# Kernel tuning notes

Hardware: AMD Instinct MI355X
Metric: run time of the kernel (lower is better)

## Reference

```python
import jax, jax.numpy as jnp
import numpy as np

B, S, D = 1, 2048, 2048
HQ, HKV, DH = 16, 4, 128
WINDOW = 512  # sliding window encoded in explicit attn_mask


def rotate_half(u):
    u1, u2 = jnp.split(u, 2, axis=-1)
    return jnp.concatenate([-u2, u1], axis=-1)


def setup_inputs() -> dict:
    key = jax.random.key(0)
    ks = jax.random.split(key, 6)
    x = jax.random.normal(ks[0], (B, S, D), dtype=jnp.float32)
    # RoPE caches (standard rotary frequencies, full d_head with duplicated halves)
    pos = jnp.arange(S)
    inv_freq = 1.0 / (10000.0 ** (jnp.arange(0, DH, 2, dtype=jnp.float32) / DH))
    ang = pos[:, None].astype(jnp.float32) * inv_freq[None, :]  # [S, DH/2]
    emb = jnp.concatenate([ang, ang], axis=-1)                  # [S, DH]
    cos_cache = jnp.cos(emb)
    sin_cache = jnp.sin(emb)
    # sliding-window causal mask: attend to j<=i and i-j < WINDOW
    i = jnp.arange(S)[:, None]
    j = jnp.arange(S)[None, :]
    attn_mask = (j <= i) & ((i - j) < WINDOW)
    sc = 0.02
    Wq = jax.random.normal(ks[1], (D, HQ * DH), dtype=jnp.float32) * sc
    Wk = jax.random.normal(ks[2], (D, HKV * DH), dtype=jnp.float32) * sc
    Wv = jax.random.normal(ks[3], (D, HKV * DH), dtype=jnp.float32) * sc
    Wo = jax.random.normal(ks[4], (HQ * DH, D), dtype=jnp.float32) * sc
    return {"x": x, "cos_cache": cos_cache, "sin_cache": sin_cache,
            "positions": pos.astype(jnp.int64), "attn_mask": attn_mask,
            "Wq": Wq, "Wk": Wk, "Wv": Wv, "Wo": Wo}


def reference(x, cos_cache, sin_cache, positions, attn_mask, Wq, Wk, Wv, Wo):
    batch, seq_len, _ = x.shape
    Q = (x @ Wq).reshape(batch, seq_len, HQ, DH).transpose(0, 2, 1, 3)   # [B,HQ,S,DH]
    K = (x @ Wk).reshape(batch, seq_len, HKV, DH).transpose(0, 2, 1, 3)  # [B,HKV,S,DH]
    V = (x @ Wv).reshape(batch, seq_len, HKV, DH).transpose(0, 2, 1, 3)
    # RoPE
    cos = cos_cache[positions][None, None, :, :]  # [1,1,S,DH]
    sin = sin_cache[positions][None, None, :, :]
    Q = Q * cos + rotate_half(Q) * sin
    K = K * cos + rotate_half(K) * sin
    # GQA expansion (repeat_interleave along head dim)
    G = HQ // HKV
    K_exp = jnp.repeat(K, G, axis=1)  # [B,HQ,S,DH]
    V_exp = jnp.repeat(V, G, axis=1)
    scores = jnp.einsum('bhqd,bhkd->bhqk', Q, K_exp) / jnp.sqrt(jnp.float32(DH))
    neg_inf = jnp.finfo(scores.dtype).min
    scores = jnp.where(attn_mask[None, None, :, :], scores, neg_inf)
    weights = jax.nn.softmax(scores, axis=-1)
    attn_out = jnp.einsum('bhqk,bhkd->bhqd', weights, V_exp)
    attn_out = attn_out.transpose(0, 2, 1, 3).reshape(batch, seq_len, HQ * DH)
    output = attn_out @ Wo
    return (output, K, V)  # new kv cache is the (post-RoPE) K, V
```

## Files before the change

kernel.cpp:

```cpp
#include <hip/hip_runtime.h>
#include <stdint.h>

typedef unsigned short u16;
typedef __attribute__((ext_vector_type(4))) float f32x4;
typedef __attribute__((ext_vector_type(8))) short short8;
typedef __attribute__((ext_vector_type(4))) short short4v;

__device__ inline u16 f2bf(float f) {
  union { float f; uint32_t u; } v; v.f = f;
  uint32_t u = v.u;
  u += 0x7fffu + ((u >> 16) & 1u);
  return (u16)(u >> 16);
}
__device__ inline float bf2f(u16 b) {
  union { uint32_t u; float f; } v; v.u = (uint32_t)b << 16; return v.f;
}

__global__ __launch_bounds__(256) void k_prep(const float* __restrict__ x,
                                              const float* __restrict__ Wq, const float* __restrict__ Wk,
                                              const float* __restrict__ Wv, const float* __restrict__ Wo,
                                              u16* __restrict__ xb, u16* __restrict__ WT, u16* __restrict__ WoT) {
  const int b = blockIdx.x, tid = threadIdx.x;
  if (b < 1024) {
    size_t base = (size_t)b * 4096 + tid * 4;
    #pragma unroll
    for (int k = 0; k < 4; ++k) {
      f32x4 v = *(const f32x4*)(x + base + k * 1024);
      short4v o;
      o.x = (short)f2bf(v.x); o.y = (short)f2bf(v.y);
      o.z = (short)f2bf(v.z); o.w = (short)f2bf(v.w);
      *(short4v*)(xb + base + k * 1024) = o;
    }
    return;
  }
  __shared__ float t[64][68];
  const float* W; u16* D; int N, bb;
  if (b < 2048)      { W = Wq; D = WT;                       N = 2048; bb = b - 1024; }
  else if (b < 2304) { W = Wk; D = WT + (size_t)2048 * 2048; N = 512;  bb = b - 2048; }
  else if (b < 2560) { W = Wv; D = WT + (size_t)2560 * 2048; N = 512;  bb = b - 2304; }
  else               { W = Wo; D = WoT;                      N = 2048; bb = b - 2560; }
  const int nb = N >> 6;
  const int n0 = (bb % nb) * 64, k0 = (bb / nb) * 64;
  const int c4 = (tid & 15) * 4, rbase = tid >> 4;
  #pragma unroll
  for (int p = 0; p < 4; ++p) {
    int r = p * 16 + rbase;
    *(f32x4*)&t[r][c4] = *(const f32x4*)&W[(size_t)(k0 + r) * N + n0 + c4];
  }
  __syncthreads();
  const int i = tid >> 2, j = (tid & 3) * 16;
  short8 o0, o1;
  #pragma unroll
  for (int m = 0; m < 8; ++m) o0[m] = (short)f2bf(t[j + m][i]);
  #pragma unroll
  for (int m = 0; m < 8; ++m) o1[m] = (short)f2bf(t[j + 8 + m][i]);
  *(short8*)&D[(size_t)(n0 + i) * 2048 + k0 + j] = o0;
  *(short8*)&D[(size_t)(n0 + i) * 2048 + k0 + j + 8] = o1;
}

__global__ __launch_bounds__(512, 2) void k_gemmqkv(const u16* __restrict__ A,
                                                    const u16* __restrict__ B,
                                                    u16* __restrict__ C) {
  const int K = 2048;
  const int NT = 32;
  __shared__ __align__(16) u16 lds[3 * 20480];
  const int tid = threadIdx.x;
  const int wid = tid >> 6, lane = tid & 63;
  const int quad = lane >> 4, l16 = lane & 15;
  const int wm = (wid >> 2) * 64;
  const int wn = (wid & 3) * 48;
  const int bm = blockIdx.y * 128, bn = blockIdx.x * 192;

  const u16* aSrc[2]; int aDst[2];
  #pragma unroll
  for (int L = 0; L < 2; ++L) {
    int E = (tid + L * 512) * 8;
    int r = E >> 6, pc = (E >> 3) & 7;
    int lc = pc ^ (r & 7);
    aSrc[L] = A + (size_t)(bm + r) * K + lc * 8;
    aDst[L] = E;
  }
  const u16* bSrc[3]; int bDst[3];
  #pragma unroll
  for (int L = 0; L < 3; ++L) {
    int E = (tid + L * 512) * 8;
    int r = E >> 6, pc = (E >> 3) & 7;
    int lc = pc ^ (r & 7);
    bSrc[L] = B + (size_t)(bn + r) * K + lc * 8;
    bDst[L] = 8192 + E;
  }

  #define STAGE(buf, kt) do {                                                              \
    _Pragma("unroll")                                                                      \
    for (int L = 0; L < 2; ++L)                                                            \
      __builtin_amdgcn_global_load_lds(                                                    \
          (const __attribute__((address_space(1))) void*)(aSrc[L] + (kt) * 64),            \
          (__attribute__((address_space(3))) void*)(&lds[(buf) * 20480 + aDst[L]]), 16, 0, 0); \
    _Pragma("unroll")                                                                      \
    for (int L = 0; L < 3; ++L)                                                            \
      __builtin_amdgcn_global_load_lds(                                                    \
          (const __attribute__((address_space(1))) void*)(bSrc[L] + (kt) * 64),            \
          (__attribute__((address_space(3))) void*)(&lds[(buf) * 20480 + bDst[L]]), 16, 0, 0); \
  } while (0)

  f32x4 acc[4][3];
  #pragma unroll
  for (int m = 0; m < 4; ++m)
    #pragma unroll
    for (int n = 0; n < 3; ++n) acc[m][n] = (f32x4){0.f, 0.f, 0.f, 0.f};

  STAGE(0, 0);
  STAGE(1, 1);
  asm volatile("s_waitcnt vmcnt(5)" ::: "memory");
  __builtin_amdgcn_s_barrier();

  int c = 0, p = 2;
  for (int t = 0; t < NT; ++t) {
    if (t + 2 < NT) STAGE(p, t + 2);

    short8 af[4][2], bf[3][2];
    #pragma unroll
    for (int mf = 0; mf < 4; ++mf)
      #pragma unroll
      for (int kc = 0; kc < 2; ++kc) {
        int R = wm + mf * 16 + l16;
        int pc = (kc * 4 + quad) ^ (R & 7);
        af[mf][kc] = *(const short8*)&lds[c * 20480 + R * 64 + pc * 8];
      }
    #pragma unroll
    for (int nf = 0; nf < 3; ++nf)
      #pragma unroll
      for (int kc = 0; kc < 2; ++kc) {
        int Cc = wn + nf * 16 + l16;
        int pc = (kc * 4 + quad) ^ (Cc & 7);
        bf[nf][kc] = *(const short8*)&lds[c * 20480 + 8192 + Cc * 64 + pc * 8];
      }

    __builtin_amdgcn_s_setprio(1);
    #pragma unroll
    for (int mf = 0; mf < 4; ++mf)
      #pragma unroll
      for (int nf = 0; nf < 3; ++nf)
        #pragma unroll
        for (int kc = 0; kc < 2; ++kc)
          acc[mf][nf] = __builtin_amdgcn_mfma_f32_16x16x32_bf16(af[mf][kc], bf[nf][kc], acc[mf][nf], 0, 0, 0);
    __builtin_amdgcn_s_setprio(0);

    if (t + 2 < NT) {
      asm volatile("s_waitcnt vmcnt(5)" ::: "memory");
    } else if (t + 1 < NT) {
      asm volatile("s_waitcnt vmcnt(0)" ::: "memory");
    }
    __builtin_amdgcn_s_barrier();
    c = (c == 2) ? 0 : c + 1;
    p = (p == 2) ? 0 : p + 1;
  }
  #undef STAGE

  #pragma unroll
  for (int mf = 0; mf < 4; ++mf) {
    int row = bm + wm + mf * 16 + quad * 4;
    #pragma unroll
    for (int nf = 0; nf < 3; ++nf) {
      int col = bn + wn + nf * 16 + l16;
      #pragma unroll
      for (int r = 0; r < 4; ++r)
        C[(size_t)(row + r) * 3072 + col] = f2bf(acc[mf][nf][r]);
    }
  }
}

__global__ __launch_bounds__(512, 2) void k_gemmo(const u16* __restrict__ A,
                                                  const u16* __restrict__ B,
                                                  float* __restrict__ C) {
  const int K = 2048;
  const int NT = 32;
  __shared__ __align__(16) u16 lds[3 * 16384];
  const int tid = threadIdx.x;
  const int wid = tid >> 6, lane = tid & 63;
  const int quad = lane >> 4, l16 = lane & 15;
  const int wm = (wid >> 2) * 64;
  const int wn = (wid & 3) * 32;
  const int bm = blockIdx.y * 128, bn = blockIdx.x * 128;

  const u16* aSrc[2]; const u16* bSrc[2]; int dDst[2];
  #pragma unroll
  for (int L = 0; L < 2; ++L) {
    int E = (tid + L * 512) * 8;
    int r = E >> 6, pc = (E >> 3) & 7;
    int lc = pc ^ (r & 7);
    aSrc[L] = A + (size_t)(bm + r) * K + lc * 8;
    bSrc[L] = B + (size_t)(bn + r) * K + lc * 8;
    dDst[L] = E;
  }

  #define STAGEO(buf, kt) do {                                                             \
    _Pragma("unroll")                                                                      \
    for (int L = 0; L < 2; ++L)                                                            \
      __builtin_amdgcn_global_load_lds(                                                    \
          (const __attribute__((address_space(1))) void*)(aSrc[L] + (kt) * 64),            \
          (__attribute__((address_space(3))) void*)(&lds[(buf) * 16384 + dDst[L]]), 16, 0, 0); \
    _Pragma("unroll")                                                                      \
    for (int L = 0; L < 2; ++L)                                                            \
      __builtin_amdgcn_global_load_lds(                                                    \
          (const __attribute__((address_space(1))) void*)(bSrc[L] + (kt) * 64),            \
          (__attribute__((address_space(3))) void*)(&lds[(buf) * 16384 + 8192 + dDst[L]]), 16, 0, 0); \
  } while (0)

  f32x4 acc[4][2];
  #pragma unroll
  for (int m = 0; m < 4; ++m)
    #pragma unroll
    for (int n = 0; n < 2; ++n) acc[m][n] = (f32x4){0.f, 0.f, 0.f, 0.f};

  STAGEO(0, 0);
  STAGEO(1, 1);
  asm volatile("s_waitcnt vmcnt(4)" ::: "memory");
  __builtin_amdgcn_s_barrier();

  int c = 0, p = 2;
  for (int t = 0; t < NT; ++t) {
    if (t + 2 < NT) STAGEO(p, t + 2);

    short8 af[4][2], bf[2][2];
    #pragma unroll
    for (int mf = 0; mf < 4; ++mf)
      #pragma unroll
      for (int kc = 0; kc < 2; ++kc) {
        int R = wm + mf * 16 + l16;
        int pc = (kc * 4 + quad) ^ (R & 7);
        af[mf][kc] = *(const short8*)&lds[c * 16384 + R * 64 + pc * 8];
      }
    #pragma unroll
    for (int nf = 0; nf < 2; ++nf)
      #pragma unroll
      for (int kc = 0; kc < 2; ++kc) {
        int Cc = wn + nf * 16 + l16;
        int pc = (kc * 4 + quad) ^ (Cc & 7);
        bf[nf][kc] = *(const short8*)&lds[c * 16384 + 8192 + Cc * 64 + pc * 8];
      }

    __builtin_amdgcn_s_setprio(1);
    #pragma unroll
    for (int mf = 0; mf < 4; ++mf)
      #pragma unroll
      for (int nf = 0; nf < 2; ++nf)
        #pragma unroll
        for (int kc = 0; kc < 2; ++kc)
          acc[mf][nf] = __builtin_amdgcn_mfma_f32_16x16x32_bf16(af[mf][kc], bf[nf][kc], acc[mf][nf], 0, 0, 0);
    __builtin_amdgcn_s_setprio(0);

    if (t + 2 < NT) {
      asm volatile("s_waitcnt vmcnt(4)" ::: "memory");
    } else if (t + 1 < NT) {
      asm volatile("s_waitcnt vmcnt(0)" ::: "memory");
    }
    __builtin_amdgcn_s_barrier();
    c = (c == 2) ? 0 : c + 1;
    p = (p == 2) ? 0 : p + 1;
  }
  #undef STAGEO

  #pragma unroll
  for (int mf = 0; mf < 4; ++mf) {
    int row = bm + wm + mf * 16 + quad * 4;
    #pragma unroll
    for (int nf = 0; nf < 2; ++nf) {
      int col = bn + wn + nf * 16 + l16;
      #pragma unroll
      for (int r = 0; r < 4; ++r)
        C[(size_t)(row + r) * 2048 + col] = acc[mf][nf][r];
    }
  }
}

__global__ __launch_bounds__(256) void k_post(const u16* __restrict__ P,
                                              const float* __restrict__ cosc, const float* __restrict__ sinc,
                                              u16* __restrict__ Qb, u16* __restrict__ Kb, u16* __restrict__ Vt,
                                              float* __restrict__ Kout, float* __restrict__ Vout) {
  const int b = blockIdx.x, tid = threadIdx.x;
  if (b < 2048) {
    __shared__ float row[3072];
    const int s = b;
    const u16* p0 = P + (size_t)s * 3072;
    for (int i = tid * 4; i < 3072; i += 1024) {
      short4v a0 = *(const short4v*)(p0 + i);
      #pragma unroll
      for (int m = 0; m < 4; ++m)
        row[i + m] = bf2f((u16)a0[m]);
    }
    __syncthreads();
    const int d = tid & 127;
    const int hbase = tid >> 7;
    const float c = cosc[s * 128 + d], sn = sinc[s * 128 + d];
    const float scale = 0.08838834764831845f;
    #pragma unroll
    for (int it = 0; it < 12; ++it) {
      int slice = it * 2 + hbase;
      float v = row[slice * 128 + d];
      if (slice < 20) {
        float other = (d < 64) ? -row[slice * 128 + d + 64] : row[slice * 128 + d - 64];
        float r = v * c + other * sn;
        if (slice < 16) {
          Qb[((size_t)slice * 2048 + s) * 128 + d] = f2bf(r * scale);
        } else {
          int hk = slice - 16;
          Kout[((size_t)hk * 2048 + s) * 128 + d] = r;
          Kb[((size_t)hk * 2048 + s) * 128 + d] = f2bf(r);
        }
      } else {
        int hv = slice - 20;
        Vout[((size_t)hv * 2048 + s) * 128 + d] = v;
      }
    }
  } else {
    __shared__ float t[32][33];
    const int b2 = b - 2048;
    const int c0 = (b2 & 15) * 32, s0 = (b2 >> 4) * 32;
    const int tx = tid & 31, ty = tid >> 5;
    #pragma unroll
    for (int i = ty; i < 32; i += 8) {
      size_t idx = (size_t)(s0 + i) * 3072 + 2560 + c0 + tx;
      t[i][tx] = bf2f(P[idx]);
    }
    __syncthreads();
    const int head = c0 >> 7, dbase = c0 & 127;
    #pragma unroll
    for (int i = ty; i < 32; i += 8)
      Vt[((size_t)head * 128 + dbase + i) * 2048 + s0 + tx] = f2bf(t[tx][i]);
  }
}

__global__ __launch_bounds__(512) void k_attn(const u16* __restrict__ Qb,
                                              const u16* __restrict__ Kb,
                                              const u16* __restrict__ Vt,
                                              u16* __restrict__ O) {
  const int qt = blockIdx.x;
  const int hk = blockIdx.y;
  const int tid = threadIdx.x;
  const int wid = tid >> 6, lane = tid & 63;
  const int quad = lane >> 4, l16 = lane & 15;
  const int h = hk * 4 + (wid >> 1);
  const int qrow0 = qt * 32;
  const int r0 = qrow0 + (wid & 1) * 16;
  const u16* Qh = Qb + (size_t)h * 2048 * 128;
  const u16* Kh = Kb + (size_t)hk * 2048 * 128;
  const u16* Vh = Vt + (size_t)hk * 128 * 2048;

  __shared__ u16 Ks[32 * 136];
  __shared__ u16 Vs[128 * 40];
  __shared__ u16 Ps[8][16 * 40];

  short8 qa[4];
  #pragma unroll
  for (int ks = 0; ks < 4; ++ks)
    qa[ks] = *(const short8*)&Qh[(size_t)(r0 + l16) * 128 + ks * 32 + quad * 8];

  f32x4 o[8];
  #pragma unroll
  for (int dt = 0; dt < 8; ++dt) o[dt] = (f32x4){0.f, 0.f, 0.f, 0.f};
  float lsum[4] = {0.f, 0.f, 0.f, 0.f};

  const int c0 = qrow0 > 511 ? (qrow0 - 511) >> 5 : 0;
  const int c1 = (qrow0 + 31) >> 5;

  short8 kreg, vreg;
  {
    const int jb = c0 * 32;
    kreg = *(const short8*)&Kh[(size_t)(jb + (tid >> 4)) * 128 + (tid & 15) * 8];
    vreg = *(const short8*)&Vh[(size_t)(tid >> 2) * 2048 + jb + (tid & 3) * 8];
  }

  for (int c = c0; c <= c1; ++c) {
    const int jbase = c * 32;
    __syncthreads();
    *(short8*)&Ks[(tid >> 4) * 136 + (tid & 15) * 8] = kreg;
    *(short8*)&Vs[(tid >> 2) * 40  + (tid & 3)  * 8] = vreg;
    if (c < c1) {
      const int jb = jbase + 32;
      kreg = *(const short8*)&Kh[(size_t)(jb + (tid >> 4)) * 128 + (tid & 15) * 8];
      vreg = *(const short8*)&Vh[(size_t)(tid >> 2) * 2048 + jb + (tid & 3) * 8];
    }
    __syncthreads();

    f32x4 sc[2];
    #pragma unroll
    for (int ni = 0; ni < 2; ++ni) {
      sc[ni] = (f32x4){0.f, 0.f, 0.f, 0.f};
      #pragma unroll
      for (int ks = 0; ks < 4; ++ks) {
        short8 kf = *(const short8*)&Ks[(ni * 16 + l16) * 136 + ks * 32 + quad * 8];
        sc[ni] = __builtin_amdgcn_mfma_f32_16x16x32_bf16(qa[ks], kf, sc[ni], 0, 0, 0);
      }
    }
    #pragma unroll
    for (int ni = 0; ni < 2; ++ni) {
      const int jlo = jbase + ni * 16;
      const bool none = (jlo > r0 + 15) || (jlo + 15 < r0 - 511);
      const bool allv = (jlo + 15 <= r0) && (jlo >= r0 - 496);
      float p[4];
      if (none) {
        p[0] = p[1] = p[2] = p[3] = 0.f;
      } else if (allv) {
        #pragma unroll
        for (int r = 0; r < 4; ++r) p[r] = __expf(sc[ni][r]);
      } else {
        const int j = jlo + l16;
        #pragma unroll
        for (int r = 0; r < 4; ++r) {
          int i = r0 + quad * 4 + r;
          bool ok = (j <= i) && (i - j < 512);
          p[r] = ok ? __expf(sc[ni][r]) : 0.f;
        }
      }
      #pragma unroll
      for (int r = 0; r < 4; ++r) {
        lsum[r] += p[r];
        Ps[wid][(quad * 4 + r) * 40 + ni * 16 + l16] = f2bf(p[r]);
      }
    }
    short8 pa = *(const short8*)&Ps[wid][l16 * 40 + quad * 8];
    #pragma unroll
    for (int dt = 0; dt < 8; ++dt) {
      short8 vf = *(const short8*)&Vs[(dt * 16 + l16) * 40 + quad * 8];
      o[dt] = __builtin_amdgcn_mfma_f32_16x16x32_bf16(pa, vf, o[dt], 0, 0, 0);
    }
  }

  #pragma unroll
  for (int off = 1; off < 16; off <<= 1)
    #pragma unroll
    for (int r = 0; r < 4; ++r)
      lsum[r] += __shfl_xor(lsum[r], off, 64);
  float inv[4];
  #pragma unroll
  for (int r = 0; r < 4; ++r) inv[r] = 1.0f / lsum[r];

  #pragma unroll
  for (int dt = 0; dt < 8; ++dt) {
    int col = h * 128 + dt * 16 + l16;
    #pragma unroll
    for (int r = 0; r < 4; ++r) {
      int row = r0 + quad * 4 + r;
      O[(size_t)row * 2048 + col] = f2bf(o[dt][r] * inv[r]);
    }
  }
}

extern "C" void kernel_launch(void* const* d_in, const int* in_sizes, int n_in,
                              void* d_out, int out_size, void* d_ws, size_t ws_size,
                              hipStream_t stream) {
  const float* x    = (const float*)d_in[0];
  const float* cosc = (const float*)d_in[1];
  const float* sinc = (const float*)d_in[2];
  const float* Wq = (const float*)d_in[5];
  const float* Wk = (const float*)d_in[6];
  const float* Wv = (const float*)d_in[7];
  const float* Wo = (const float*)d_in[8];

  char* ws = (char*)d_ws;
  u16*   xb    = (u16*)(ws);
  u16*   O     = (u16*)(ws);
  u16*   WT    = (u16*)(ws + (8u  << 20));
  u16*   WoT   = (u16*)(ws + (20u << 20));
  u16*   Qb    = (u16*)(ws + (28u << 20));
  u16*   Kb    = (u16*)(ws + (36u << 20));
  u16*   Vt    = (u16*)(ws + (38u << 20));
  u16*   QKV   = (u16*)(ws + (40u << 20));

  float* outO = (float*)d_out;
  float* outK = (float*)d_out + 4194304;
  float* outV = (float*)d_out + 5242880;

  k_prep<<<3584, 256, 0, stream>>>(x, Wq, Wk, Wv, Wo, xb, WT, WoT);
  k_gemmqkv<<<dim3(16, 16), 512, 0, stream>>>(xb, WT, QKV);
  k_post<<<3072, 256, 0, stream>>>(QKV, cosc, sinc, Qb, Kb, Vt, outK, outV);
  k_attn<<<dim3(64, 4), 512, 0, stream>>>(Qb, Kb, Vt, O);
  k_gemmo<<<dim3(16, 16), 512, 0, stream>>>(O, WoT, outO);
}
```

Measured before the change: 102.4 us.

## Retile output GEMM to 4 waves with BK=32 and double attention KV chunk

The output-projection GEMM moves from 8 waves with a 64-wide K step to 4 waves, each computing a 64x64 tile over a 32-wide K step with a re-derived LDS swizzle. This halves LDS use and increases per-wave register reuse, but doubles the number of barriers and pipeline iterations. Separately, the attention kernel processes 64 keys per chunk instead of 32, halving the number of synchronised load/compute iterations. The cost is more registers and LDS per block and more masked work at the window edges.

```diff
diff --git a/kernel.cpp b/kernel.cpp
--- a/kernel.cpp
+++ b/kernel.cpp
@@ -170,25 +170,24 @@
   }
 }
 
-__global__ __launch_bounds__(512, 2) void k_gemmo(const u16* __restrict__ A,
-                                                  const u16* __restrict__ B,
-                                                  float* __restrict__ C) {
+__global__ __launch_bounds__(256) void k_gemmo(const u16* __restrict__ A,
+                                               const u16* __restrict__ B,
+                                               float* __restrict__ C) {
   const int K = 2048;
-  const int NT = 32;
-  __shared__ __align__(16) u16 lds[3 * 16384];
+  const int NT = 64;
+  __shared__ __align__(16) u16 lds[3 * 8192];
   const int tid = threadIdx.x;
   const int wid = tid >> 6, lane = tid & 63;
   const int quad = lane >> 4, l16 = lane & 15;
-  const int wm = (wid >> 2) * 64;
-  const int wn = (wid & 3) * 32;
+  const int wm = (wid >> 1) * 64, wn = (wid & 1) * 64;
   const int bm = blockIdx.y * 128, bn = blockIdx.x * 128;
 
   const u16* aSrc[2]; const u16* bSrc[2]; int dDst[2];
   #pragma unroll
   for (int L = 0; L < 2; ++L) {
-    int E = (tid + L * 512) * 8;
-    int r = E >> 6, pc = (E >> 3) & 7;
-    int lc = pc ^ (r & 7);
+    int E = (tid + L * 256) * 8;
+    int r = E >> 5, pc = (E >> 3) & 3;
+    int lc = pc ^ ((r >> 1) & 3);
     aSrc[L] = A + (size_t)(bm + r) * K + lc * 8;
     bSrc[L] = B + (size_t)(bn + r) * K + lc * 8;
     dDst[L] = E;
@@ -198,20 +197,20 @@
     _Pragma("unroll")                                                                      \
     for (int L = 0; L < 2; ++L)                                                            \
       __builtin_amdgcn_global_load_lds(                                                    \
-          (const __attribute__((address_space(1))) void*)(aSrc[L] + (kt) * 64),            \
-          (__attribute__((address_space(3))) void*)(&lds[(buf) * 16384 + dDst[L]]), 16, 0, 0); \
+          (const __attribute__((address_space(1))) void*)(aSrc[L] + (kt) * 32),            \
+          (__attribute__((address_space(3))) void*)(&lds[(buf) * 8192 + dDst[L]]), 16, 0, 0); \
     _Pragma("unroll")                                                                      \
     for (int L = 0; L < 2; ++L)                                                            \
       __builtin_amdgcn_global_load_lds(                                                    \
-          (const __attribute__((address_space(1))) void*)(bSrc[L] + (kt) * 64),            \
-          (__attribute__((address_space(3))) void*)(&lds[(buf) * 16384 + 8192 + dDst[L]]), 16, 0, 0); \
+          (const __attribute__((address_space(1))) void*)(bSrc[L] + (kt) * 32),            \
+          (__attribute__((address_space(3))) void*)(&lds[(buf) * 8192 + 4096 + dDst[L]]), 16, 0, 0); \
   } while (0)
 
-  f32x4 acc[4][2];
+  f32x4 acc[4][4];
   #pragma unroll
   for (int m = 0; m < 4; ++m)
     #pragma unroll
-    for (int n = 0; n < 2; ++n) acc[m][n] = (f32x4){0.f, 0.f, 0.f, 0.f};
+    for (int n = 0; n < 4; ++n) acc[m][n] = (f32x4){0.f, 0.f, 0.f, 0.f};
 
   STAGEO(0, 0);
   STAGEO(1, 1);
@@ -222,32 +221,26 @@
   for (int t = 0; t < NT; ++t) {
     if (t + 2 < NT) STAGEO(p, t + 2);
 
-    short8 af[4][2], bf[2][2];
+    short8 af[4], bf[4];
+    #pragma unroll
+    for (int mf = 0; mf < 4; ++mf) {
+      int R = wm + mf * 16 + l16;
+      int pc = quad ^ ((R >> 1) & 3);
+      af[mf] = *(const short8*)&lds[c * 8192 + R * 32 + pc * 8];
+    }
+    #pragma unroll
+    for (int nf = 0; nf < 4; ++nf) {
+      int Cc = wn + nf * 16 + l16;
+      int pc = quad ^ ((Cc >> 1) & 3);
+      bf[nf] = *(const short8*)&lds[c * 8192 + 4096 + Cc * 32 + pc * 8];
+    }
+
+    __builtin_amdgcn_s_setprio(1);
     #pragma unroll
     for (int mf = 0; mf < 4; ++mf)
       #pragma unroll
-      for (int kc = 0; kc < 2; ++kc) {
-        int R = wm + mf * 16 + l16;
-        int pc = (kc * 4 + quad) ^ (R & 7);
-        af[mf][kc] = *(const short8*)&lds[c * 16384 + R * 64 + pc * 8];
-      }
-    #pragma unroll
-    for (int nf = 0; nf < 2; ++nf)
-      #pragma unroll
-      for (int kc = 0; kc < 2; ++kc) {
-        int Cc = wn + nf * 16 + l16;
-        int pc = (kc * 4 + quad) ^ (Cc & 7);
-        bf[nf][kc] = *(const short8*)&lds[c * 16384 + 8192 + Cc * 64 + pc * 8];
-      }
-
-    __builtin_amdgcn_s_setprio(1);
-    #pragma unroll
-    for (int mf = 0; mf < 4; ++mf)
-      #pragma unroll
-      for (int nf = 0; nf < 2; ++nf)
-        #pragma unroll
-        for (int kc = 0; kc < 2; ++kc)
-          acc[mf][nf] = __builtin_amdgcn_mfma_f32_16x16x32_bf16(af[mf][kc], bf[nf][kc], acc[mf][nf], 0, 0, 0);
+      for (int nf = 0; nf < 4; ++nf)
+        acc[mf][nf] = __builtin_amdgcn_mfma_f32_16x16x32_bf16(af[mf], bf[nf], acc[mf][nf], 0, 0, 0);
     __builtin_amdgcn_s_setprio(0);
 
     if (t + 2 < NT) {
@@ -265,7 +258,7 @@
   for (int mf = 0; mf < 4; ++mf) {
     int row = bm + wm + mf * 16 + quad * 4;
     #pragma unroll
-    for (int nf = 0; nf < 2; ++nf) {
+    for (int nf = 0; nf < 4; ++nf) {
       int col = bn + wn + nf * 16 + l16;
       #pragma unroll
       for (int r = 0; r < 4; ++r)
@@ -347,9 +340,9 @@
   const u16* Kh = Kb + (size_t)hk * 2048 * 128;
   const u16* Vh = Vt + (size_t)hk * 128 * 2048;
 
-  __shared__ u16 Ks[32 * 136];
-  __shared__ u16 Vs[128 * 40];
-  __shared__ u16 Ps[8][16 * 40];
+  __shared__ u16 Ks[64 * 136];
+  __shared__ u16 Vs[128 * 72];
+  __shared__ u16 Ps[8][16 * 72];
 
   short8 qa[4];
   #pragma unroll
@@ -361,31 +354,43 @@
   for (int dt = 0; dt < 8; ++dt) o[dt] = (f32x4){0.f, 0.f, 0.f, 0.f};
   float lsum[4] = {0.f, 0.f, 0.f, 0.f};
 
-  const int c0 = qrow0 > 511 ? (qrow0 - 511) >> 5 : 0;
-  const int c1 = (qrow0 + 31) >> 5;
-
-  short8 kreg, vreg;
+  const int c0 = qrow0 > 511 ? (qrow0 - 511) >> 6 : 0;
+  const int c1 = (qrow0 + 31) >> 6;
+
+  short8 kreg[2], vreg[2];
   {
-    const int jb = c0 * 32;
-    kreg = *(const short8*)&Kh[(size_t)(jb + (tid >> 4)) * 128 + (tid & 15) * 8];
-    vreg = *(const short8*)&Vh[(size_t)(tid >> 2) * 2048 + jb + (tid & 3) * 8];
+    const int jb = c0 * 64;
+    #pragma unroll
+    for (int i = 0; i < 2; ++i) {
+      int lin = i * 512 + tid;
+      kreg[i] = *(const short8*)&Kh[(size_t)(jb + (lin >> 4)) * 128 + (lin & 15) * 8];
+      vreg[i] = *(const short8*)&Vh[(size_t)(lin >> 3) * 2048 + jb + (lin & 7) * 8];
+    }
   }
 
   for (int c = c0; c <= c1; ++c) {
-    const int jbase = c * 32;
+    const int jbase = c * 64;
     __syncthreads();
-    *(short8*)&Ks[(tid >> 4) * 136 + (tid & 15) * 8] = kreg;
-    *(short8*)&Vs[(tid >> 2) * 40  + (tid & 3)  * 8] = vreg;
+    #pragma unroll
+    for (int i = 0; i < 2; ++i) {
+      int lin = i * 512 + tid;
+      *(short8*)&Ks[(lin >> 4) * 136 + (lin & 15) * 8] = kreg[i];
+      *(short8*)&Vs[(lin >> 3) * 72  + (lin & 7)  * 8] = vreg[i];
+    }
     if (c < c1) {
-      const int jb = jbase + 32;
-      kreg = *(const short8*)&Kh[(size_t)(jb + (tid >> 4)) * 128 + (tid & 15) * 8];
-      vreg = *(const short8*)&Vh[(size_t)(tid >> 2) * 2048 + jb + (tid & 3) * 8];
+      const int jb = jbase + 64;
+      #pragma unroll
+      for (int i = 0; i < 2; ++i) {
+        int lin = i * 512 + tid;
+        kreg[i] = *(const short8*)&Kh[(size_t)(jb + (lin >> 4)) * 128 + (lin & 15) * 8];
+        vreg[i] = *(const short8*)&Vh[(size_t)(lin >> 3) * 2048 + jb + (lin & 7) * 8];
+      }
     }
     __syncthreads();
 
-    f32x4 sc[2];
-    #pragma unroll
-    for (int ni = 0; ni < 2; ++ni) {
+    f32x4 sc[4];
+    #pragma unroll
+    for (int ni = 0; ni < 4; ++ni) {
       sc[ni] = (f32x4){0.f, 0.f, 0.f, 0.f};
       #pragma unroll
       for (int ks = 0; ks < 4; ++ks) {
@@ -394,7 +399,7 @@
       }
     }
     #pragma unroll
-    for (int ni = 0; ni < 2; ++ni) {
+    for (int ni = 0; ni < 4; ++ni) {
       const int jlo = jbase + ni * 16;
       const bool none = (jlo > r0 + 15) || (jlo + 15 < r0 - 511);
       const bool allv = (jlo + 15 <= r0) && (jlo >= r0 - 496);
@@ -416,14 +421,20 @@
       #pragma unroll
       for (int r = 0; r < 4; ++r) {
         lsum[r] += p[r];
-        Ps[wid][(quad * 4 + r) * 40 + ni * 16 + l16] = f2bf(p[r]);
-      }
-    }
-    short8 pa = *(const short8*)&Ps[wid][l16 * 40 + quad * 8];
+        Ps[wid][(quad * 4 + r) * 72 + ni * 16 + l16] = f2bf(p[r]);
+      }
+    }
+    short8 pa[2];
+    #pragma unroll
+    for (int kc = 0; kc < 2; ++kc)
+      pa[kc] = *(const short8*)&Ps[wid][l16 * 72 + kc * 32 + quad * 8];
     #pragma unroll
     for (int dt = 0; dt < 8; ++dt) {
-      short8 vf = *(const short8*)&Vs[(dt * 16 + l16) * 40 + quad * 8];
-      o[dt] = __builtin_amdgcn_mfma_f32_16x16x32_bf16(pa, vf, o[dt], 0, 0, 0);
+      #pragma unroll
+      for (int kc = 0; kc < 2; ++kc) {
+        short8 vf = *(const short8*)&Vs[(dt * 16 + l16) * 72 + kc * 32 + quad * 8];
+        o[dt] = __builtin_amdgcn_mfma_f32_16x16x32_bf16(pa[kc], vf, o[dt], 0, 0, 0);
+      }
     }
   }
 
@@ -476,5 +487,5 @@
   k_gemmqkv<<<dim3(16, 16), 512, 0, stream>>>(xb, WT, QKV);
   k_post<<<3072, 256, 0, stream>>>(QKV, cosc, sinc, Qb, Kb, Vt, outK, outV);
   k_attn<<<dim3(64, 4), 512, 0, stream>>>(Qb, Kb, Vt, O);
-  k_gemmo<<<dim3(16, 16), 512, 0, stream>>>(O, WoT, outO);
-}
+  k_gemmo<<<dim3(16, 16), 256, 0, stream>>>(O, WoT, outO);
+}
```

Result: slower. 111.1 us (+8.4%).

## Split K across two warp groups in QKV GEMM with LDS reduction

Applied to the files above, without the earlier changes.

The QKV projection GEMM now splits each 64-wide K step into two 32-wide halves, each handled by a group of four warps. Each warp computes a larger 64x96 output tile, which cuts LDS fragment reads per MFMA. The two partial accumulators are summed through LDS in an epilogue. This doubles accumulator registers per warp and adds a reduction phase with extra barriers, which may affect occupancy.

```diff
diff --git a/kernel.cpp b/kernel.cpp
--- a/kernel.cpp
+++ b/kernel.cpp
@@ -62,111 +62,122 @@
                                                     const u16* __restrict__ B,
                                                     u16* __restrict__ C) {
   const int K = 2048;
-  const int NT = 32;
-  __shared__ __align__(16) u16 lds[3 * 20480];
+  const int NIT = 32;
+  __shared__ __align__(16) u16 lds[6 * 10240];
   const int tid = threadIdx.x;
   const int wid = tid >> 6, lane = tid & 63;
   const int quad = lane >> 4, l16 = lane & 15;
-  const int wm = (wid >> 2) * 64;
-  const int wn = (wid & 3) * 48;
+  const int kg = wid >> 2;
+  const int wl = wid & 3;
+  const int wm = (wl >> 1) * 64, wn = (wl & 1) * 96;
   const int bm = blockIdx.y * 128, bn = blockIdx.x * 192;
 
-  const u16* aSrc[2]; int aDst[2];
-  #pragma unroll
-  for (int L = 0; L < 2; ++L) {
-    int E = (tid + L * 512) * 8;
-    int r = E >> 6, pc = (E >> 3) & 7;
-    int lc = pc ^ (r & 7);
-    aSrc[L] = A + (size_t)(bm + r) * K + lc * 8;
-    aDst[L] = E;
-  }
-  const u16* bSrc[3]; int bDst[3];
-  #pragma unroll
-  for (int L = 0; L < 3; ++L) {
-    int E = (tid + L * 512) * 8;
-    int r = E >> 6, pc = (E >> 3) & 7;
-    int lc = pc ^ (r & 7);
-    bSrc[L] = B + (size_t)(bn + r) * K + lc * 8;
-    bDst[L] = 8192 + E;
-  }
-
-  #define STAGE(buf, kt) do {                                                              \
-    _Pragma("unroll")                                                                      \
-    for (int L = 0; L < 2; ++L)                                                            \
-      __builtin_amdgcn_global_load_lds(                                                    \
-          (const __attribute__((address_space(1))) void*)(aSrc[L] + (kt) * 64),            \
-          (__attribute__((address_space(3))) void*)(&lds[(buf) * 20480 + aDst[L]]), 16, 0, 0); \
-    _Pragma("unroll")                                                                      \
-    for (int L = 0; L < 3; ++L)                                                            \
-      __builtin_amdgcn_global_load_lds(                                                    \
-          (const __attribute__((address_space(1))) void*)(bSrc[L] + (kt) * 64),            \
-          (__attribute__((address_space(3))) void*)(&lds[(buf) * 20480 + bDst[L]]), 16, 0, 0); \
+  const u16 *sA0, *sB0, *sB1, *sBx;
+  int dA0, dB0, dB1, dBx, xodd;
+  {
+    int s, r, pc, lc;
+    s = tid;       r = s >> 2; pc = s & 3; lc = pc ^ ((r >> 1) & 3);
+    sA0 = A + (size_t)(bm + r) * K + lc * 8; dA0 = s * 8;
+    sB0 = B + (size_t)(bn + r) * K + lc * 8; dB0 = 4096 + s * 8;
+    s = tid + 256; r = s >> 2; pc = s & 3; lc = pc ^ ((r >> 1) & 3);
+    sB1 = B + (size_t)(bn + r) * K + lc * 8; dB1 = 4096 + s * 8;
+    if (tid < 256) { s = 512 + tid; xodd = 0; } else { s = tid - 256; xodd = 1; }
+    r = s >> 2; pc = s & 3; lc = pc ^ ((r >> 1) & 3);
+    sBx = B + (size_t)(bn + r) * K + lc * 8; dBx = 4096 + s * 8;
+  }
+
+  #define GLDS(src, dst) __builtin_amdgcn_global_load_lds(                                 \
+      (const __attribute__((address_space(1))) void*)(src),                                \
+      (__attribute__((address_space(3))) void*)(dst), 16, 0, 0)
+  #define STAGE(be, j) do {                                                                \
+    GLDS(sA0 + (2 * (j)) * 32,        &lds[(be) * 10240 + dA0]);                           \
+    GLDS(sB0 + (2 * (j)) * 32,        &lds[(be) * 10240 + dB0]);                           \
+    GLDS(sA0 + (2 * (j) + 1) * 32,    &lds[((be) + 1) * 10240 + dA0]);                     \
+    GLDS(sB1 + (2 * (j) + 1) * 32,    &lds[((be) + 1) * 10240 + dB1]);                     \
+    GLDS(sBx + (2 * (j) + xodd) * 32, &lds[((be) + xodd) * 10240 + dBx]);                  \
   } while (0)
 
-  f32x4 acc[4][3];
+  f32x4 acc[4][6];
   #pragma unroll
   for (int m = 0; m < 4; ++m)
     #pragma unroll
-    for (int n = 0; n < 3; ++n) acc[m][n] = (f32x4){0.f, 0.f, 0.f, 0.f};
+    for (int n = 0; n < 6; ++n) acc[m][n] = (f32x4){0.f, 0.f, 0.f, 0.f};
 
   STAGE(0, 0);
-  STAGE(1, 1);
+  STAGE(2, 1);
   asm volatile("s_waitcnt vmcnt(5)" ::: "memory");
   __builtin_amdgcn_s_barrier();
 
-  int c = 0, p = 2;
-  for (int t = 0; t < NT; ++t) {
-    if (t + 2 < NT) STAGE(p, t + 2);
-
-    short8 af[4][2], bf[3][2];
+  int cb = 0, sb = 4;
+  for (int it = 0; it < NIT; ++it) {
+    if (it + 2 < NIT) STAGE(sb, it + 2);
+
+    const u16* Lb = &lds[(cb + kg) * 10240];
+    short8 af[4], bfr[6];
+    #pragma unroll
+    for (int mf = 0; mf < 4; ++mf) {
+      int R = wm + mf * 16 + l16;
+      int pc = quad ^ ((R >> 1) & 3);
+      af[mf] = *(const short8*)&Lb[R * 32 + pc * 8];
+    }
+    #pragma unroll
+    for (int nf = 0; nf < 6; ++nf) {
+      int Cc = wn + nf * 16 + l16;
+      int pc = quad ^ ((Cc >> 1) & 3);
+      bfr[nf] = *(const short8*)&Lb[4096 + Cc * 32 + pc * 8];
+    }
+
+    __builtin_amdgcn_s_setprio(1);
     #pragma unroll
     for (int mf = 0; mf < 4; ++mf)
       #pragma unroll
-      for (int kc = 0; kc < 2; ++kc) {
-        int R = wm + mf * 16 + l16;
-        int pc = (kc * 4 + quad) ^ (R & 7);
-        af[mf][kc] = *(const short8*)&lds[c * 20480 + R * 64 + pc * 8];
-      }
-    #pragma unroll
-    for (int nf = 0; nf < 3; ++nf)
-      #pragma unroll
-      for (int kc = 0; kc < 2; ++kc) {
-        int Cc = wn + nf * 16 + l16;
-        int pc = (kc * 4 + quad) ^ (Cc & 7);
-        bf[nf][kc] = *(const short8*)&lds[c * 20480 + 8192 + Cc * 64 + pc * 8];
-      }
-
-    __builtin_amdgcn_s_setprio(1);
-    #pragma unroll
-    for (int mf = 0; mf < 4; ++mf)
-      #pragma unroll
-      for (int nf = 0; nf < 3; ++nf)
+      for (int nf = 0; nf < 6; ++nf)
+        acc[mf][nf] = __builtin_amdgcn_mfma_f32_16x16x32_bf16(af[mf], bfr[nf], acc[mf][nf], 0, 0, 0);
+    __builtin_amdgcn_s_setprio(0);
+
+    if (it + 2 < NIT) {
+      asm volatile("s_waitcnt vmcnt(5)" ::: "memory");
+    } else if (it + 1 < NIT) {
+      asm volatile("s_waitcnt vmcnt(0)" ::: "memory");
+    }
+    __builtin_amdgcn_s_barrier();
+    cb = (cb == 4) ? 0 : cb + 2;
+    sb = (sb == 4) ? 0 : sb + 2;
+  }
+  #undef STAGE
+  #undef GLDS
+
+  __syncthreads();
+  float* red = (float*)lds;
+  #pragma unroll
+  for (int ch = 0; ch < 3; ++ch) {
+    if (kg == 1) {
+      #pragma unroll
+      for (int mf = 0; mf < 4; ++mf)
         #pragma unroll
-        for (int kc = 0; kc < 2; ++kc)
-          acc[mf][nf] = __builtin_amdgcn_mfma_f32_16x16x32_bf16(af[mf][kc], bf[nf][kc], acc[mf][nf], 0, 0, 0);
-    __builtin_amdgcn_s_setprio(0);
-
-    if (t + 2 < NT) {
-      asm volatile("s_waitcnt vmcnt(5)" ::: "memory");
-    } else if (t + 1 < NT) {
-      asm volatile("s_waitcnt vmcnt(0)" ::: "memory");
-    }
-    __builtin_amdgcn_s_barrier();
-    c = (c == 2) ? 0 : c + 1;
-    p = (p == 2) ? 0 : p + 1;
-  }
-  #undef STAGE
-
-  #pragma unroll
-  for (int mf = 0; mf < 4; ++mf) {
-    int row = bm + wm + mf * 16 + quad * 4;
-    #pragma unroll
-    for (int nf = 0; nf < 3; ++nf) {
-      int col = bn + wn + nf * 16 + l16;
-      #pragma unroll
-      for (int r = 0; r < 4; ++r)
-        C[(size_t)(row + r) * 3072 + col] = f2bf(acc[mf][nf][r]);
-    }
+        for (int j = 0; j < 2; ++j)
+          #pragma unroll
+          for (int r = 0; r < 4; ++r)
+            red[wl * 2048 + (mf * 2 + j) * 256 + r * 64 + lane] = acc[mf][ch * 2 + j][r];
+    }
+    __syncthreads();
+    if (kg == 0) {
+      #pragma unroll
+      for (int mf = 0; mf < 4; ++mf) {
+        int row = bm + wm + mf * 16 + quad * 4;
+        #pragma unroll
+        for (int j = 0; j < 2; ++j) {
+          int nf = ch * 2 + j;
+          int col = bn + wn + nf * 16 + l16;
+          #pragma unroll
+          for (int r = 0; r < 4; ++r) {
+            float s = acc[mf][nf][r] + red[wl * 2048 + (mf * 2 + j) * 256 + r * 64 + lane];
+            C[(size_t)(row + r) * 3072 + col] = f2bf(s);
+          }
+        }
+      }
+    }
+    __syncthreads();
   }
 }
 
```

Measured after the change: 105.8 us. 3.3% more time.

## Split attention KV tiles across warp pairs with shared-memory reduction of partials

Applied to the files above, without the earlier changes.

Each warp now processes all 32 query rows of its head and only every other 32-key tile. Two key/value tiles are staged per iteration, so the number of block-wide barriers per key span is halved and each K/V fragment read feeds two MFMAs. The partial outputs and row sums from the two warps of each head are combined through shared memory at the end. This costs extra registers for the doubled accumulators and a larger shared-memory footprint, which may lower occupancy.

```diff
diff --git a/kernel.cpp b/kernel.cpp
--- a/kernel.cpp
+++ b/kernel.cpp
@@ -340,110 +340,197 @@
   const int tid = threadIdx.x;
   const int wid = tid >> 6, lane = tid & 63;
   const int quad = lane >> 4, l16 = lane & 15;
-  const int h = hk * 4 + (wid >> 1);
+  const int hq = wid >> 1;
+  const int kg = wid & 1;
+  const int h = hk * 4 + hq;
   const int qrow0 = qt * 32;
-  const int r0 = qrow0 + (wid & 1) * 16;
   const u16* Qh = Qb + (size_t)h * 2048 * 128;
   const u16* Kh = Kb + (size_t)hk * 2048 * 128;
   const u16* Vh = Vt + (size_t)hk * 128 * 2048;
 
-  __shared__ u16 Ks[32 * 136];
-  __shared__ u16 Vs[128 * 40];
-  __shared__ u16 Ps[8][16 * 40];
-
-  short8 qa[4];
-  #pragma unroll
-  for (int ks = 0; ks < 4; ++ks)
-    qa[ks] = *(const short8*)&Qh[(size_t)(r0 + l16) * 128 + ks * 32 + quad * 8];
-
-  f32x4 o[8];
-  #pragma unroll
-  for (int dt = 0; dt < 8; ++dt) o[dt] = (f32x4){0.f, 0.f, 0.f, 0.f};
-  float lsum[4] = {0.f, 0.f, 0.f, 0.f};
-
-  const int c0 = qrow0 > 511 ? (qrow0 - 511) >> 5 : 0;
-  const int c1 = (qrow0 + 31) >> 5;
-
-  short8 kreg, vreg;
+  __shared__ __align__(16) char smem[58368];
+  u16* Ks = (u16*)smem;
+  u16* Vs = (u16*)(smem + 17408);
+  u16* Pw = (u16*)(smem + 37888) + wid * 1280;
+
+  short8 qa[2][4];
+  #pragma unroll
+  for (int mi = 0; mi < 2; ++mi)
+    #pragma unroll
+    for (int ks = 0; ks < 4; ++ks)
+      qa[mi][ks] = *(const short8*)&Qh[(size_t)(qrow0 + mi * 16 + l16) * 128 + ks * 32 + quad * 8];
+
+  f32x4 o[2][8];
+  #pragma unroll
+  for (int mi = 0; mi < 2; ++mi)
+    #pragma unroll
+    for (int dt = 0; dt < 8; ++dt) o[mi][dt] = (f32x4){0.f, 0.f, 0.f, 0.f};
+  float lsum[2][4] = {{0.f,0.f,0.f,0.f},{0.f,0.f,0.f,0.f}};
+
+  const int t0 = qrow0 > 511 ? (qrow0 - 511) >> 5 : 0;
+  const int t1 = (qrow0 + 31) >> 5;
+  const int tb0 = t0 & ~1;
+
+  const int krow = tid >> 4, kcol = (tid & 15) * 8;
+  const int vrow = tid >> 2, vcol = (tid & 3) * 8;
+
+  short8 kreg[2], vreg[2];
   {
-    const int jb = c0 * 32;
-    kreg = *(const short8*)&Kh[(size_t)(jb + (tid >> 4)) * 128 + (tid & 15) * 8];
-    vreg = *(const short8*)&Vh[(size_t)(tid >> 2) * 2048 + jb + (tid & 3) * 8];
-  }
-
-  for (int c = c0; c <= c1; ++c) {
-    const int jbase = c * 32;
+    int j0 = tb0 * 32;
+    int j1 = ((tb0 + 1 <= t1) ? tb0 + 1 : t1) * 32;
+    kreg[0] = *(const short8*)&Kh[(size_t)(j0 + krow) * 128 + kcol];
+    kreg[1] = *(const short8*)&Kh[(size_t)(j1 + krow) * 128 + kcol];
+    vreg[0] = *(const short8*)&Vh[(size_t)vrow * 2048 + j0 + vcol];
+    vreg[1] = *(const short8*)&Vh[(size_t)vrow * 2048 + j1 + vcol];
+  }
+
+  for (int tb = tb0; tb <= t1; tb += 2) {
     __syncthreads();
-    *(short8*)&Ks[(tid >> 4) * 136 + (tid & 15) * 8] = kreg;
-    *(short8*)&Vs[(tid >> 2) * 40  + (tid & 3)  * 8] = vreg;
-    if (c < c1) {
-      const int jb = jbase + 32;
-      kreg = *(const short8*)&Kh[(size_t)(jb + (tid >> 4)) * 128 + (tid & 15) * 8];
-      vreg = *(const short8*)&Vh[(size_t)(tid >> 2) * 2048 + jb + (tid & 3) * 8];
+    *(short8*)&Ks[0 * 4352 + krow * 136 + kcol] = kreg[0];
+    *(short8*)&Ks[1 * 4352 + krow * 136 + kcol] = kreg[1];
+    *(short8*)&Vs[0 * 5120 + vrow * 40 + vcol] = vreg[0];
+    *(short8*)&Vs[1 * 5120 + vrow * 40 + vcol] = vreg[1];
+    if (tb + 2 <= t1) {
+      int j0 = (tb + 2) * 32;
+      int j1 = ((tb + 3 <= t1) ? tb + 3 : t1) * 32;
+      kreg[0] = *(const short8*)&Kh[(size_t)(j0 + krow) * 128 + kcol];
+      kreg[1] = *(const short8*)&Kh[(size_t)(j1 + krow) * 128 + kcol];
+      vreg[0] = *(const short8*)&Vh[(size_t)vrow * 2048 + j0 + vcol];
+      vreg[1] = *(const short8*)&Vh[(size_t)vrow * 2048 + j1 + vcol];
     }
     __syncthreads();
 
-    f32x4 sc[2];
+    const int tt = tb + kg;
+    if (tt < t0 || tt > t1) continue;
+    const u16* Kss = Ks + kg * 4352;
+    const u16* Vss = Vs + kg * 5120;
+    const int jbase = tt * 32;
+
+    f32x4 sc[2][2];
     #pragma unroll
     for (int ni = 0; ni < 2; ++ni) {
-      sc[ni] = (f32x4){0.f, 0.f, 0.f, 0.f};
+      sc[0][ni] = (f32x4){0.f, 0.f, 0.f, 0.f};
+      sc[1][ni] = (f32x4){0.f, 0.f, 0.f, 0.f};
       #pragma unroll
       for (int ks = 0; ks < 4; ++ks) {
-        short8 kf = *(const short8*)&Ks[(ni * 16 + l16) * 136 + ks * 32 + quad * 8];
-        sc[ni] = __builtin_amdgcn_mfma_f32_16x16x32_bf16(qa[ks], kf, sc[ni], 0, 0, 0);
-      }
-    }
-    #pragma unroll
-    for (int ni = 0; ni < 2; ++ni) {
-      const int jlo = jbase + ni * 16;
-      const bool none = (jlo > r0 + 15) || (jlo + 15 < r0 - 511);
-      const bool allv = (jlo + 15 <= r0) && (jlo >= r0 - 496);
-      float p[4];
-      if (none) {
-        p[0] = p[1] = p[2] = p[3] = 0.f;
-      } else if (allv) {
-        #pragma unroll
-        for (int r = 0; r < 4; ++r) p[r] = __expf(sc[ni][r]);
-      } else {
-        const int j = jlo + l16;
+        short8 kf = *(const short8*)&Kss[(ni * 16 + l16) * 136 + ks * 32 + quad * 8];
+        sc[0][ni] = __builtin_amdgcn_mfma_f32_16x16x32_bf16(qa[0][ks], kf, sc[0][ni], 0, 0, 0);
+        sc[1][ni] = __builtin_amdgcn_mfma_f32_16x16x32_bf16(qa[1][ks], kf, sc[1][ni], 0, 0, 0);
+      }
+    }
+    #pragma unroll
+    for (int mi = 0; mi < 2; ++mi) {
+      const int rlo = qrow0 + mi * 16;
+      #pragma unroll
+      for (int ni = 0; ni < 2; ++ni) {
+        const int jlo = jbase + ni * 16;
+        const bool none = (jlo > rlo + 15) || (jlo + 15 < rlo - 511);
+        const bool allv = (jlo + 15 <= rlo) && (jlo >= rlo - 496);
+        float p[4];
+        if (none) {
+          p[0] = p[1] = p[2] = p[3] = 0.f;
+        } else if (allv) {
+          #pragma unroll
+          for (int r = 0; r < 4; ++r) p[r] = __expf(sc[mi][ni][r]);
+        } else {
+          const int j = jlo + l16;
+          #pragma unroll
+          for (int r = 0; r < 4; ++r) {
+            int i = rlo + quad * 4 + r;
+            bool ok = (j <= i) && (i - j < 512);
+            p[r] = ok ? __expf(sc[mi][ni][r]) : 0.f;
+          }
+        }
         #pragma unroll
         for (int r = 0; r < 4; ++r) {
-          int i = r0 + quad * 4 + r;
-          bool ok = (j <= i) && (i - j < 512);
-          p[r] = ok ? __expf(sc[ni][r]) : 0.f;
+          lsum[mi][r] += p[r];
+          Pw[(mi * 16 + quad * 4 + r) * 40 + ni * 16 + l16] = f2bf(p[r]);
         }
       }
-      #pragma unroll
-      for (int r = 0; r < 4; ++r) {
-        lsum[r] += p[r];
-        Ps[wid][(quad * 4 + r) * 40 + ni * 16 + l16] = f2bf(p[r]);
-      }
-    }
-    short8 pa = *(const short8*)&Ps[wid][l16 * 40 + quad * 8];
+    }
+    short8 pa[2];
+    #pragma unroll
+    for (int mi = 0; mi < 2; ++mi)
+      pa[mi] = *(const short8*)&Pw[(mi * 16 + l16) * 40 + quad * 8];
     #pragma unroll
     for (int dt = 0; dt < 8; ++dt) {
-      short8 vf = *(const short8*)&Vs[(dt * 16 + l16) * 40 + quad * 8];
-      o[dt] = __builtin_amdgcn_mfma_f32_16x16x32_bf16(pa, vf, o[dt], 0, 0, 0);
+      short8 vf = *(const short8*)&Vss[(dt * 16 + l16) * 40 + quad * 8];
+      o[0][dt] = __builtin_amdgcn_mfma_f32_16x16x32_bf16(pa[0], vf, o[0][dt], 0, 0, 0);
+      o[1][dt] = __builtin_amdgcn_mfma_f32_16x16x32_bf16(pa[1], vf, o[1][dt], 0, 0, 0);
     }
   }
 
   #pragma unroll
   for (int off = 1; off < 16; off <<= 1)
     #pragma unroll
-    for (int r = 0; r < 4; ++r)
-      lsum[r] += __shfl_xor(lsum[r], off, 64);
-  float inv[4];
-  #pragma unroll
-  for (int r = 0; r < 4; ++r) inv[r] = 1.0f / lsum[r];
-
-  #pragma unroll
-  for (int dt = 0; dt < 8; ++dt) {
-    int col = h * 128 + dt * 16 + l16;
-    #pragma unroll
-    for (int r = 0; r < 4; ++r) {
-      int row = r0 + quad * 4 + r;
-      O[(size_t)row * 2048 + col] = f2bf(o[dt][r] * inv[r]);
-    }
+    for (int mi = 0; mi < 2; ++mi)
+      #pragma unroll
+      for (int r = 0; r < 4; ++r)
+        lsum[mi][r] += __shfl_xor(lsum[mi][r], off, 64);
+
+  float* redO = (float*)smem;
+  float* redL = (float*)(smem + 32768);
+  const int rbase = (hq * 64 + lane) * 32;
+  float inv[2][4];
+
+  __syncthreads();
+  if (kg == 1) {
+    #pragma unroll
+    for (int mi = 0; mi < 2; ++mi) {
+      #pragma unroll
+      for (int dt = 0; dt < 4; ++dt)
+        #pragma unroll
+        for (int r = 0; r < 4; ++r)
+          redO[rbase + mi * 16 + dt * 4 + r] = o[mi][dt][r];
+      #pragma unroll
+      for (int r = 0; r < 4; ++r)
+        redL[(hq * 64 + lane) * 8 + mi * 4 + r] = lsum[mi][r];
+    }
+  }
+  __syncthreads();
+  if (kg == 0) {
+    #pragma unroll
+    for (int mi = 0; mi < 2; ++mi)
+      #pragma unroll
+      for (int r = 0; r < 4; ++r)
+        inv[mi][r] = 1.0f / (lsum[mi][r] + redL[(hq * 64 + lane) * 8 + mi * 4 + r]);
+    #pragma unroll
+    for (int mi = 0; mi < 2; ++mi)
+      #pragma unroll
+      for (int dt = 0; dt < 4; ++dt) {
+        int col = h * 128 + dt * 16 + l16;
+        #pragma unroll
+        for (int r = 0; r < 4; ++r) {
+          int row = qrow0 + mi * 16 + quad * 4 + r;
+          float v = o[mi][dt][r] + redO[rbase + mi * 16 + dt * 4 + r];
+          O[(size_t)row * 2048 + col] = f2bf(v * inv[mi][r]);
+        }
+      }
+  }
+  __syncthreads();
+  if (kg == 1) {
+    #pragma unroll
+    for (int mi = 0; mi < 2; ++mi)
+      #pragma unroll
+      for (int dt = 4; dt < 8; ++dt)
+        #pragma unroll
+        for (int r = 0; r < 4; ++r)
+          redO[rbase + mi * 16 + (dt - 4) * 4 + r] = o[mi][dt][r];
+  }
+  __syncthreads();
+  if (kg == 0) {
+    #pragma unroll
+    for (int mi = 0; mi < 2; ++mi)
+      #pragma unroll
+      for (int dt = 4; dt < 8; ++dt) {
+        int col = h * 128 + dt * 16 + l16;
+        #pragma unroll
+        for (int r = 0; r < 4; ++r) {
+          int row = qrow0 + mi * 16 + quad * 4 + r;
+          float v = o[mi][dt][r] + redO[rbase + mi * 16 + (dt - 4) * 4 + r];
+          O[(size_t)row * 2048 + col] = f2bf(v * inv[mi][r]);
+        }
+      }
   }
 }
 
```

Measured after the change: 104.7 us. 1.02x slower.
